# Optimization experiments

Hardware: AMD Instinct MI355X
Metric: run time of the kernel (lower is better)

The kernel has to match this reference:

```python
import jax, jax.numpy as jnp
import numpy as np

B, H, W, C = 2, 48, 48, 768
HEADS, HD = 12, 64
MLP = 3072
BOT = 384


def ln(x, w, b, eps=1e-5):
    mu = x.mean(-1, keepdims=True)
    var = ((x - mu) ** 2).mean(-1, keepdims=True)
    return (x - mu) * jax.lax.rsqrt(var + eps) * w + b


def ln_chan(x, w, b, eps=1e-6):
    # detectron2-style LayerNorm over channel dim for NCHW tensors
    mu = x.mean(1, keepdims=True)
    var = ((x - mu) ** 2).mean(1, keepdims=True)
    return (x - mu) * jax.lax.rsqrt(var + eps) * w[None, :, None, None] + b[None, :, None, None]


def conv(x, w, pad):
    return jax.lax.conv_general_dilated(x, w, (1, 1), [(pad, pad), (pad, pad)],
                                        dimension_numbers=('NCHW', 'OIHW', 'NCHW'))


def setup_inputs() -> dict:
    key = jax.random.key(0)
    ks = jax.random.split(key, 32)
    r = lambda i, shape, s=0.02: (jax.random.normal(ks[i], shape) * s).astype(jnp.float32)
    return {
        'x': jax.random.normal(ks[0], (B, H, W, C), dtype=jnp.float32),
        'norm1_w': jnp.ones((C,), jnp.float32), 'norm1_b': jnp.zeros((C,), jnp.float32),
        'qkv_w': r(1, (C, 3 * C)), 'qkv_b': r(2, (3 * C,)),
        'proj_w': r(3, (C, C)), 'proj_b': r(4, (C,)),
        'rel_pos_h': r(5, (2 * H - 1, HD)), 'rel_pos_w': r(6, (2 * W - 1, HD)),
        'norm2_w': jnp.ones((C,), jnp.float32), 'norm2_b': jnp.zeros((C,), jnp.float32),
        'fc1_w': r(7, (C, MLP)), 'fc1_b': r(8, (MLP,)),
        'fc2_w': r(9, (MLP, C)), 'fc2_b': r(10, (C,)),
        'conv1_w': r(11, (BOT, C, 1, 1)), 'rln1_w': jnp.ones((BOT,), jnp.float32), 'rln1_b': jnp.zeros((BOT,), jnp.float32),
        'conv2_w': r(12, (BOT, BOT, 3, 3)), 'rln2_w': jnp.ones((BOT,), jnp.float32), 'rln2_b': jnp.zeros((BOT,), jnp.float32),
        'conv3_w': r(13, (C, BOT, 1, 1)), 'rln3_w': r(14, (C,)), 'rln3_b': r(15, (C,)),
    }


def reference(x, norm1_w, norm1_b, qkv_w, qkv_b, proj_w, proj_b, rel_pos_h, rel_pos_w,
              norm2_w, norm2_b, fc1_w, fc1_b, fc2_w, fc2_b,
              conv1_w, rln1_w, rln1_b, conv2_w, rln2_w, rln2_b, conv3_w, rln3_w, rln3_b):
    b, h, w, c = x.shape
    hd = c // HEADS
    n = h * w
    scale = hd ** -0.5

    shortcut = x
    xn = ln(x, norm1_w, norm1_b)
    # qkv projection: (B,N,3,heads,hd) -> (3, B*heads, N, hd)
    qkv = (xn.reshape(b, n, c) @ qkv_w + qkv_b).reshape(b, n, 3, HEADS, hd)
    qkv = qkv.transpose(2, 0, 3, 1, 4).reshape(3, b * HEADS, n, hd)
    q, k, v = qkv[0], qkv[1], qkv[2]

    attn = jnp.einsum('bnd,bmd->bnm', q * scale, k)  # (B*heads, N, N)

    # decomposed relative position bias
    idx_h = jnp.arange(h)[:, None] - jnp.arange(h)[None, :] + (h - 1)
    idx_w = jnp.arange(w)[:, None] - jnp.arange(w)[None, :] + (w - 1)
    Rh = rel_pos_h[idx_h]  # (H, H, hd)
    Rw = rel_pos_w[idx_w]  # (W, W, hd)
    rq = q.reshape(b * HEADS, h, w, hd)
    rel_h = jnp.einsum('bhwc,hkc->bhwk', rq, Rh)
    rel_w = jnp.einsum('bhwc,wkc->bhwk', rq, Rw)
    attn = attn.reshape(b * HEADS, h, w, h, w) + rel_h[:, :, :, :, None] + rel_w[:, :, :, None, :]
    attn = jax.nn.softmax(attn.reshape(b * HEADS, n, n), axis=-1)

    out = (attn @ v).reshape(b, HEADS, h, w, hd).transpose(0, 2, 3, 1, 4).reshape(b, h, w, c)
    x = shortcut + (out @ proj_w + proj_b)

    # MLP
    xn = ln(x, norm2_w, norm2_b)
    hdn = jax.nn.gelu(xn @ fc1_w + fc1_b, approximate=False)
    x = x + (hdn @ fc2_w + fc2_b)

    # residual bottleneck block (NCHW)
    y = x.transpose(0, 3, 1, 2)
    o = jax.nn.gelu(ln_chan(conv(y, conv1_w, 0), rln1_w, rln1_b), approximate=False)
    o = jax.nn.gelu(ln_chan(conv(o, conv2_w, 1), rln2_w, rln2_b), approximate=False)
    o = ln_chan(conv(o, conv3_w, 0), rln3_w, rln3_b)
    y = y + o
    return y.transpose(0, 2, 3, 1)
```

## Files before the change

### kernel.cpp

```cpp
#include <hip/hip_runtime.h>

typedef unsigned short ushort_t;
typedef __attribute__((ext_vector_type(8))) short bf16x8;
typedef __attribute__((ext_vector_type(4))) float f32x4;

#define DEV static __device__ __forceinline__

DEV ushort_t f2bf(float f){
  union { float f; unsigned u; } v; v.f = f;
  unsigned r = v.u + 0x7FFFu + ((v.u >> 16) & 1u);
  return (ushort_t)(r >> 16);
}
DEV float bf2f(ushort_t h){
  union { unsigned u; float f; } v; v.u = ((unsigned)h) << 16;
  return v.f;
}
DEV float gelu_f(float x){ return 0.5f * x * (1.f + erff(x * 0.70710678118654752f)); }

#define MFMA16(a,b,c) __builtin_amdgcn_mfma_f32_16x16x32_bf16((a),(b),(c),0,0,0)

DEV void gld16(const ushort_t* g, ushort_t* l){
  __builtin_amdgcn_global_load_lds(
      (const __attribute__((address_space(1))) unsigned int*)g,
      (__attribute__((address_space(3))) unsigned int*)l, 16, 0, 0);
}


__global__ __launch_bounds__(256) void transpose_all_kernel(
    const float* __restrict__ s0, const float* __restrict__ s1,
    const float* __restrict__ s2, const float* __restrict__ s3,
    ushort_t* __restrict__ d0, ushort_t* __restrict__ d1,
    ushort_t* __restrict__ d2, ushort_t* __restrict__ d3){
  __shared__ float tile[32][33];
  int b = blockIdx.x;
  const float* src; ushort_t* dst; int K, N, bx, by;
  if(b < 1728){ src=s0; dst=d0; K=768;  N=2304; bx=b%24;          by=b/24; }
  else if(b < 2304){ int c=b-1728; src=s1; dst=d1; K=768;  N=768;  bx=c%24; by=c/24; }
  else if(b < 4608){ int c=b-2304; src=s2; dst=d2; K=768;  N=3072; bx=c%24; by=c/24; }
  else             { int c=b-4608; src=s3; dst=d3; K=3072; N=768;  bx=c%96; by=c/96; }
  int k0 = bx*32, n0 = by*32;
  int tx = threadIdx.x & 31, ty = threadIdx.x >> 5;
  #pragma unroll
  for(int i = ty; i < 32; i += 8) tile[i][tx] = src[(long)(k0+i)*N + n0 + tx];
  __syncthreads();
  #pragma unroll
  for(int i = ty; i < 32; i += 8) dst[(long)(n0+i)*K + k0 + tx] = f2bf(tile[tx][i]);
}

__global__ void cast_all_kernel(
    const float* __restrict__ c1w, const float* __restrict__ c2w,
    const float* __restrict__ c3w, const float* __restrict__ rph,
    const float* __restrict__ rpw,
    ushort_t* __restrict__ wc1, ushort_t* __restrict__ wc2,
    ushort_t* __restrict__ wc3, ushort_t* __restrict__ tabh,
    ushort_t* __restrict__ tabw){
  int i = blockIdx.x*256 + threadIdx.x;
  if(i < 294912){ wc1[i] = f2bf(c1w[i]); }
  else if(i < 1622016){
    int j = i - 294912;
    int co = j / 3456, r = j - co*3456;
    int dy = r / 1152; int r2 = r - dy*1152;
    int dx = r2 / 384; int ci = r2 - dx*384;
    wc2[j] = f2bf(c2w[((co*384 + ci)*3 + dy)*3 + dx]);
  }
  else if(i < 1916928){ int j = i - 1622016; wc3[j] = f2bf(c3w[j]); }
  else if(i < 1923008){ int j = i - 1916928; tabh[j] = f2bf(rph[j]); }
  else if(i < 1929088){ int j = i - 1923008; tabw[j] = f2bf(rpw[j]); }
}

__global__ __launch_bounds__(256) void vt_kernel(
    const ushort_t* __restrict__ v, ushort_t* __restrict__ vt){
  __shared__ __align__(16) ushort_t t[64][72];
  int bh = blockIdx.y, nt = blockIdx.x;
  int tid = threadIdx.x;
  #pragma unroll
  for(int p=0;p<2;p++){
    int item = tid + p*256;
    int tok = item >> 3, ch = item & 7;
    bf16x8 vv = *(const bf16x8*)(v + ((long)(bh*2304 + nt*64 + tok))*64 + ch*8);
    #pragma unroll
    for(int j=0;j<8;j++) t[ch*8+j][tok] = (ushort_t)vv[j];
  }
  __syncthreads();
  #pragma unroll
  for(int p=0;p<2;p++){
    int item = tid + p*256;
    int d = item >> 3, c2 = item & 7;
    bf16x8 rd = *(const bf16x8*)&t[d][c2*8];
    *(bf16x8*)(vt + ((long)(bh*64 + d))*2304 + nt*64 + c2*8) = rd;
  }
}

template<int D, bool GELU, bool RES, bool PADOUT>
__global__ __launch_bounds__(256) void ln_kernel(
    const float* __restrict__ in, const float* __restrict__ w, const float* __restrict__ bv,
    const float* __restrict__ res, float eps,
    ushort_t* __restrict__ outb, float* __restrict__ outf){
  constexpr int PER = D/64;
  int lane = threadIdx.x & 63, wid = threadIdx.x >> 6;
  long row = (long)blockIdx.x*4 + wid;
  const float* ip = in + row*D;
  float x[PER]; float s = 0.f;
  #pragma unroll
  for(int i=0;i<PER;i++){ x[i] = ip[i*64 + lane]; s += x[i]; }
  #pragma unroll
  for(int o=32;o>=1;o>>=1) s += __shfl_xor(s, o);
  float mu = s * (1.f/D);
  float vs = 0.f;
  #pragma unroll
  for(int i=0;i<PER;i++){ float d = x[i]-mu; vs += d*d; }
  #pragma unroll
  for(int o=32;o>=1;o>>=1) vs += __shfl_xor(vs, o);
  float rstd = rsqrtf(vs*(1.f/D) + eps);
  long obase;
  if constexpr(PADOUT){
    int bb = (int)(row / 2304); int rm = (int)(row - (long)bb*2304);
    int y = rm / 48, xx = rm - y*48;
    obase = ((long)((bb*50 + y+1)*50) + (xx+1))*384;
  } else obase = row*D;
  #pragma unroll
  for(int i=0;i<PER;i++){
    int c = i*64 + lane;
    float y = (x[i]-mu)*rstd*w[c] + bv[c];
    if constexpr(GELU) y = gelu_f(y);
    if constexpr(RES)  y += res[row*D + c];
    if(outb) outb[obase + c] = f2bf(y);
    if(outf) outf[row*D + c] = y;
  }
}

__global__ __launch_bounds__(256) void relpos_mfma_kernel(
    const ushort_t* __restrict__ q, const ushort_t* __restrict__ tabh,
    const ushort_t* __restrict__ tabw,
    float* __restrict__ relh, float* __restrict__ relw){
  const int bh = blockIdx.y;
  const bool isH = (blockIdx.z == 0);
  const int w = threadIdx.x >> 6, lane = threadIdx.x & 63;
  const int la = lane & 15, grp = lane >> 4;
  const int pos0 = blockIdx.x*4 + w;
  const ushort_t* tab = isH ? tabh : tabw;
  float* outp = isH ? relh : relw;
  const ushort_t* qbase = q + (long)bh*2304*64;

  bf16x8 bf0[3], bf1[3];
  #pragma unroll
  for(int ni=0;ni<3;ni++){
    int dpos = pos0 - (ni*16+la) + 47;
    const ushort_t* tp = tab + dpos*64 + grp*8;
    bf0[ni] = *(const bf16x8*)tp;
    bf1[ni] = *(const bf16x8*)(tp+32);
  }
  #pragma unroll
  for(int mi=0;mi<3;mi++){
    int arow = mi*16 + la;
    long na = isH ? ((long)pos0*48 + arow) : ((long)arow*48 + pos0);
    const ushort_t* qp = qbase + na*64 + grp*8;
    bf16x8 a0 = *(const bf16x8*)qp;
    bf16x8 a1 = *(const bf16x8*)(qp+32);
    f32x4 c[3];
    #pragma unroll
    for(int ni=0;ni<3;ni++){
      f32x4 z; z[0]=0.f; z[1]=0.f; z[2]=0.f; z[3]=0.f;
      z = MFMA16(a0, bf0[ni], z);
      z = MFMA16(a1, bf1[ni], z);
      c[ni] = z;
    }
    #pragma unroll
    for(int ni=0;ni<3;ni++)
      #pragma unroll
      for(int r=0;r<4;r++){
        int orow = mi*16 + grp*4 + r;
        long no = isH ? ((long)pos0*48 + orow) : ((long)orow*48 + pos0);
        outp[((long)bh*2304 + no)*48 + ni*16 + la] = c[ni][r] * 8.0f;
      }
  }
}

template<int BM, int BN, int EPI, bool IM2COL>
__global__ __launch_bounds__(256) void gemm_kernel(
    const ushort_t* __restrict__ A, const ushort_t* __restrict__ Wt,
    const float* __restrict__ bias, const float* __restrict__ res,
    float* __restrict__ outf, ushort_t* __restrict__ ob0,
    ushort_t* __restrict__ ob1, ushort_t* __restrict__ ob2,
    int N, int Kdim){
  constexpr int FRm = BM/32, FRn = BN/32;
  __shared__ __align__(16) ushort_t Asm[BM*64];
  __shared__ __align__(16) ushort_t Bsm[BN*64];
  const int tid = threadIdx.x, lane = tid & 63, w = tid >> 6;
  const int wm = w >> 1, wn = w & 1;
  const int la = lane & 15, grp = lane >> 4;
  const int m0 = blockIdx.y * BM, n0 = blockIdx.x * BN;
  f32x4 acc[FRm][FRn];
  #pragma unroll
  for(int i=0;i<FRm;i++)
    #pragma unroll
    for(int j=0;j<FRn;j++)
      #pragma unroll
      for(int r=0;r<4;r++) acc[i][j][r] = 0.f;

  const int srw = lane >> 3;
  const int scs = ((lane&7) ^ srw) * 8;
  for(int k0 = 0; k0 < Kdim; k0 += 64){
    if(k0) __syncthreads();
    #pragma unroll
    for(int t=0;t<FRm;t++){
      int r = w*(BM/4) + t*8 + srw;
      const ushort_t* ga;
      if constexpr(IM2COL){
        int m = m0 + r;
        int bb = m / 2304; int rm = m - bb*2304;
        int y = rm / 48, x = rm - y*48;
        int dy = k0 / 1152; int r2 = k0 - dy*1152;
        int dx = r2 / 384;  int cb = r2 - dx*384;
        ga = A + (((long)((bb*50 + y+dy)*50) + (x+dx))*384 + cb + scs);
      } else {
        ga = A + (long)(m0+r)*Kdim + k0 + scs;
      }
      gld16(ga, &Asm[(w*(BM/4)+t*8)*64]);
    }
    #pragma unroll
    for(int t=0;t<FRn;t++){
      int r = w*(BN/4) + t*8 + srw;
      gld16(Wt + (long)(n0+r)*Kdim + k0 + scs, &Bsm[(w*(BN/4)+t*8)*64]);
    }
    __syncthreads();
    #pragma unroll
    for(int ks=0; ks<2; ks++){
      bf16x8 af[FRm], bfm[FRn];
      #pragma unroll
      for(int mi=0;mi<FRm;mi++){
        int row = wm*(BM/2) + mi*16 + la;
        af[mi] = *(const bf16x8*)&Asm[row*64 + ((((ks<<2)+grp) ^ (row&7))*8)];
      }
      #pragma unroll
      for(int ni=0;ni<FRn;ni++){
        int row = wn*(BN/2) + ni*16 + la;
        bfm[ni] = *(const bf16x8*)&Bsm[row*64 + ((((ks<<2)+grp) ^ (row&7))*8)];
      }
      #pragma unroll
      for(int mi=0;mi<FRm;mi++)
        #pragma unroll
        for(int ni=0;ni<FRn;ni++)
          acc[mi][ni] = MFMA16(af[mi], bfm[ni], acc[mi][ni]);
    }
  }
  #pragma unroll
  for(int mi=0;mi<FRm;mi++)
  #pragma unroll
  for(int ni=0;ni<FRn;ni++)
  #pragma unroll
  for(int r=0;r<4;r++){
    int mm = m0 + wm*(BM/2) + mi*16 + grp*4 + r;
    int nn = n0 + wn*(BN/2) + ni*16 + la;
    float v = acc[mi][ni][r];
    if constexpr(EPI == 0){
      outf[(long)mm*N + nn] = v;
    } else if constexpr(EPI == 1){
      v += bias[nn];
      int s = nn / 768; int rem = nn - s*768;
      int head = rem >> 6, d = rem & 63;
      if(s == 0) v *= 0.125f;
      int bb = mm / 2304; int nloc = mm - bb*2304;
      long idx = ((long)((bb*12+head)*2304 + nloc))*64 + d;
      ushort_t hv = f2bf(v);
      if(s == 0) ob0[idx] = hv; else if(s == 1) ob1[idx] = hv; else ob2[idx] = hv;
    } else if constexpr(EPI == 2){
      v += bias[nn] + res[(long)mm*N + nn];
      outf[(long)mm*N + nn] = v;
    } else if constexpr(EPI == 3){
      v = gelu_f(v + bias[nn]);
      ob0[(long)mm*N + nn] = f2bf(v);
    } else if constexpr(EPI == 4){
      v += bias[nn] + res[(long)mm*N + nn];
      outf[(long)mm*N + nn] = v;
      ob0[(long)mm*N + nn] = f2bf(v);
    }
  }
}

#define NSPLIT 2
#define NTS 18
__global__ __launch_bounds__(512) void attn_kernel(
    const ushort_t* __restrict__ Q, const ushort_t* __restrict__ Kb,
    const ushort_t* __restrict__ VT, const float* __restrict__ relh,
    const float* __restrict__ relw, float* __restrict__ Opart,
    float* __restrict__ mpart, float* __restrict__ lpart){
  __shared__ __align__(16) ushort_t Kl[2][64*64];
  __shared__ __align__(16) ushort_t Vl[2][64*64];
  const int bh = blockIdx.y, qt = blockIdx.x, sp = blockIdx.z;
  const int tid = threadIdx.x, lane = tid & 63, w = tid >> 6;
  const int la = lane & 15, grp = lane >> 4;
  const int qg = qt*128 + w*16 + la;
  const long row = (long)bh*2304 + qg;
  const int key0 = sp*NTS*64;

  const ushort_t* qp = Q + row*64 + grp*8;
  const bf16x8 qa0 = *(const bf16x8*)qp;
  const bf16x8 qa1 = *(const bf16x8*)(qp + 32);

  const ushort_t* kg = Kb + ((long)bh*2304 + key0)*64;
  const ushort_t* vg = VT + (long)bh*64*2304 + key0;
  const float* rhq = relh + row*48;

  f32x4 rw4[3];
  {
    const float* rwq = relw + row*48 + grp*4;
    #pragma unroll
    for(int c=0;c<3;c++) rw4[c] = *(const f32x4*)(rwq + 16*c);
  }

  const int srw = lane >> 3;
  const int scs = ((lane&7) ^ srw) * 8;
  const int strow = w*8 + srw;

  f32x4 acc[4];
  #pragma unroll
  for(int nf=0;nf<4;nf++){ acc[nf][0]=0.f; acc[nf][1]=0.f; acc[nf][2]=0.f; acc[nf][3]=0.f; }
  float m_run = -3e38f, l_run = 0.f;

  gld16(kg + (long)strow*64 + scs, &Kl[0][(w*8)*64]);
  gld16(vg + (long)strow*2304 + scs, &Vl[0][(w*8)*64]);

  for(int t=0; t<6; t++){
    #define ATTN_ITER(u)                                                         \
    {                                                                            \
      const int j = 3*t + (u);                                                   \
      const int cur = (t + (u)) & 1;                                             \
      asm volatile("s_waitcnt vmcnt(0)" ::: "memory");                           \
      __builtin_amdgcn_sched_barrier(0);                                         \
      __builtin_amdgcn_s_barrier();                                              \
      __builtin_amdgcn_sched_barrier(0);                                         \
      const int h0 = sp*24 + 4*t + (u);                                          \
      const float rha = rhq[h0];                                                 \
      const float rhb = rhq[h0+1];                                               \
      if(j+1 < NTS){                                                             \
        gld16(kg + ((long)((j+1)*64 + strow))*64 + scs, &Kl[cur^1][(w*8)*64]);   \
        gld16(vg + (long)strow*2304 + (j+1)*64 + scs, &Vl[cur^1][(w*8)*64]);     \
      }                                                                          \
      f32x4 s[4];                                                                \
      _Pragma("unroll")                                                          \
      for(int nf=0;nf<4;nf++){                                                   \
        const ushort_t* kl = &Kl[cur][(nf*16+la)*64];                            \
        bf16x8 k0 = *(const bf16x8*)(kl + ((grp ^ (la&7))*8));                   \
        bf16x8 k1 = *(const bf16x8*)(kl + (((4+grp) ^ (la&7))*8));               \
        f32x4 z; z[0]=0.f; z[1]=0.f; z[2]=0.f; z[3]=0.f;                         \
        z = MFMA16(k0, qa0, z);                                                  \
        z = MFMA16(k1, qa1, z);                                                  \
        s[nf] = z;                                                               \
      }                                                                          \
      float lmax = -3e38f;                                                       \
      _Pragma("unroll")                                                          \
      for(int nf=0;nf<4;nf++){                                                   \
        const int cp = (u) + nf;                                                 \
        const float rh = (cp >= 3) ? rhb : rha;                                  \
        const int c = (cp >= 3) ? cp-3 : cp;                                     \
        _Pragma("unroll")                                                        \
        for(int r=0;r<4;r++){                                                    \
          s[nf][r] += rh + rw4[c][r];                                            \
          lmax = fmaxf(lmax, s[nf][r]);                                          \
        }                                                                        \
      }                                                                          \
      lmax = fmaxf(lmax, __shfl_xor(lmax,16));                                   \
      lmax = fmaxf(lmax, __shfl_xor(lmax,32));                                   \
      if(!__all(lmax <= m_run + 8.f)){                                           \
        const float mnew = fmaxf(m_run, lmax);                                   \
        const float alpha = __expf(m_run - mnew);                                \
        m_run = mnew;                                                            \
        l_run *= alpha;                                                          \
        _Pragma("unroll")                                                        \
        for(int nf=0;nf<4;nf++)                                                  \
          _Pragma("unroll")                                                      \
          for(int r=0;r<4;r++) acc[nf][r] *= alpha;                              \
      }                                                                          \
      float psum = 0.f;                                                          \
      _Pragma("unroll")                                                          \
      for(int nf=0;nf<4;nf++)                                                    \
        _Pragma("unroll")                                                        \
        for(int r=0;r<4;r++){                                                    \
          s[nf][r] = __expf(s[nf][r] - m_run);                                   \
          psum += s[nf][r];                                                      \
        }                                                                        \
      psum += __shfl_xor(psum,16);                                               \
      psum += __shfl_xor(psum,32);                                               \
      l_run += psum;                                                             \
      unsigned pk[4][2];                                                         \
      _Pragma("unroll")                                                          \
      for(int nf=0;nf<4;nf++)                                                    \
        _Pragma("unroll")                                                        \
        for(int h=0;h<2;h++)                                                     \
          asm("v_cvt_pk_bf16_f32 %0, %1, %2"                                     \
              : "=v"(pk[nf][h]) : "v"(s[nf][2*h]), "v"(s[nf][2*h+1]));           \
      _Pragma("unroll")                                                          \
      for(int ks=0; ks<2; ks++){                                                 \
        unsigned wd[4];                                                          \
        _Pragma("unroll")                                                        \
        for(int j2=0;j2<4;j2++){                                                 \
          int src = la + 16*(((grp&1)<<1) + (j2>>1));                            \
          unsigned wA = __shfl(pk[2*ks  ][j2&1], src);                           \
          unsigned wB = __shfl(pk[2*ks+1][j2&1], src);                           \
          wd[j2] = (grp >= 2) ? wB : wA;                                         \
        }                                                                        \
        union { unsigned uu[4]; bf16x8 v; } pa;                                  \
        pa.uu[0]=wd[0]; pa.uu[1]=wd[1]; pa.uu[2]=wd[2]; pa.uu[3]=wd[3];          \
        _Pragma("unroll")                                                        \
        for(int nf=0;nf<4;nf++){                                                 \
          const ushort_t* vl = &Vl[cur][(nf*16+la)*64];                          \
          bf16x8 vb = *(const bf16x8*)(vl + ((((ks<<2)+grp) ^ (la&7))*8));       \
          acc[nf] = MFMA16(vb, pa.v, acc[nf]);                                   \
        }                                                                        \
      }                                                                          \
    }
    ATTN_ITER(0)
    ATTN_ITER(1)
    ATTN_ITER(2)
    #undef ATTN_ITER
  }

  float* op = Opart + ((long)sp*55296 + row)*64;
  #pragma unroll
  for(int nf=0;nf<4;nf++)
    *(f32x4*)(op + nf*16 + grp*4) = acc[nf];
  if(grp == 0){
    mpart[(long)sp*55296 + row] = m_run;
    lpart[(long)sp*55296 + row] = l_run;
  }
}

__global__ __launch_bounds__(256) void attn_merge_kernel(
    const float* __restrict__ Opart, const float* __restrict__ mpart,
    const float* __restrict__ lpart, ushort_t* __restrict__ outp){
  int wid = threadIdx.x >> 6, lane = threadIdx.x & 63;
  long row = (long)blockIdx.x*4 + wid;
  int bh = (int)(row / 2304); int n = (int)(row - (long)bh*2304);
  int b = bh / 12, head = bh - b*12;
  float m0 = mpart[row], m1 = mpart[55296+row];
  float ms = fmaxf(m0, m1);
  float w0 = __expf(m0-ms), w1 = __expf(m1-ms);
  float l = w0*lpart[row] + w1*lpart[55296+row];
  float o = w0*Opart[row*64+lane] + w1*Opart[(55296+row)*64+lane];
  outp[((long)b*2304+n)*768 + head*64 + lane] = f2bf(o / l);
}

extern "C" void kernel_launch(void* const* d_in, const int* in_sizes, int n_in,
                              void* d_out, int out_size, void* d_ws, size_t ws_size,
                              hipStream_t stream){
  const float* x     = (const float*)d_in[0];
  const float* n1w   = (const float*)d_in[1];
  const float* n1b   = (const float*)d_in[2];
  const float* qkvw  = (const float*)d_in[3];
  const float* qkvb  = (const float*)d_in[4];
  const float* projw = (const float*)d_in[5];
  const float* projb = (const float*)d_in[6];
  const float* rph   = (const float*)d_in[7];
  const float* rpw   = (const float*)d_in[8];
  const float* n2w   = (const float*)d_in[9];
  const float* n2b   = (const float*)d_in[10];
  const float* fc1w  = (const float*)d_in[11];
  const float* fc1b  = (const float*)d_in[12];
  const float* fc2w  = (const float*)d_in[13];
  const float* fc2b  = (const float*)d_in[14];
  const float* c1w   = (const float*)d_in[15];
  const float* r1w   = (const float*)d_in[16];
  const float* r1b   = (const float*)d_in[17];
  const float* c2w   = (const float*)d_in[18];
  const float* r2w   = (const float*)d_in[19];
  const float* r2b   = (const float*)d_in[20];
  const float* c3w   = (const float*)d_in[21];
  const float* r3w   = (const float*)d_in[22];
  const float* r3b   = (const float*)d_in[23];
  float* out = (float*)d_out;

  char* base = (char*)d_ws;
  size_t off = 0;
  auto carve = [&](size_t bytes)->char*{
    char* p = base + off;
    off += (bytes + 255) & ~(size_t)255;
    return p;
  };
  const long T = 4608;

  ushort_t* wqkvT = (ushort_t*)carve((size_t)2304*768*2);
  ushort_t* wprojT= (ushort_t*)carve((size_t)768*768*2);
  ushort_t* wfc1T = (ushort_t*)carve((size_t)3072*768*2);
  ushort_t* wfc2T = (ushort_t*)carve((size_t)768*3072*2);
  ushort_t* wc1   = (ushort_t*)carve((size_t)384*768*2);
  ushort_t* wc2   = (ushort_t*)carve((size_t)384*3456*2);
  ushort_t* wc3   = (ushort_t*)carve((size_t)768*384*2);
  ushort_t* tabhb = (ushort_t*)carve((size_t)95*64*2);
  ushort_t* tabwb = (ushort_t*)carve((size_t)95*64*2);
  ushort_t* xn1   = (ushort_t*)carve((size_t)T*768*2);
  ushort_t* qb    = (ushort_t*)carve((size_t)24*2304*64*2);
  ushort_t* kbuf  = (ushort_t*)carve((size_t)24*2304*64*2);
  ushort_t* vbuf  = (ushort_t*)carve((size_t)24*2304*64*2);
  ushort_t* vbufT = (ushort_t*)carve((size_t)24*2304*64*2);
  float*    relh  = (float*)carve((size_t)24*2304*48*4);
  float*    relw  = (float*)carve((size_t)24*2304*48*4);
  float*    Opart = (float*)carve((size_t)2*55296*64*4);
  float*    mpart = (float*)carve((size_t)2*55296*4);
  float*    lpart = (float*)carve((size_t)2*55296*4);
  ushort_t* attno = (ushort_t*)carve((size_t)T*768*2);
  float*    x1    = (float*)carve((size_t)T*768*4);
  ushort_t* xn2   = (ushort_t*)carve((size_t)T*768*2);
  ushort_t* hmlp  = (ushort_t*)carve((size_t)T*3072*2);
  float*    x2    = (float*)carve((size_t)T*768*4);
  ushort_t* x2b   = (ushort_t*)carve((size_t)T*768*2);
  float*    c1    = (float*)carve((size_t)T*384*4);
  ushort_t* o1pad = (ushort_t*)carve((size_t)2*50*50*384*2);
  float*    c2    = (float*)carve((size_t)T*384*4);
  ushort_t* o2    = (ushort_t*)carve((size_t)T*384*2);
  float*    c3    = (float*)carve((size_t)T*768*4);
  (void)ws_size; (void)in_sizes; (void)n_in; (void)out_size;

  transpose_all_kernel<<<dim3(6912),256,0,stream>>>(qkvw, projw, fc1w, fc2w,
                                                    wqkvT, wprojT, wfc1T, wfc2T);
  cast_all_kernel<<<dim3(7536),256,0,stream>>>(c1w, c2w, c3w, rph, rpw,
                                               wc1, wc2, wc3, tabhb, tabwb);
  hipMemsetAsync(o1pad, 0, (size_t)2*50*50*384*2, stream);

  ln_kernel<768,false,false,false><<<dim3(1152),256,0,stream>>>(x, n1w, n1b, nullptr, 1e-5f, xn1, nullptr);
  gemm_kernel<128,128,1,false><<<dim3(18,36),256,0,stream>>>(xn1, wqkvT, qkvb, nullptr, nullptr, qb, kbuf, vbuf, 2304, 768);
  vt_kernel<<<dim3(36,24),256,0,stream>>>(vbuf, vbufT);
  relpos_mfma_kernel<<<dim3(12,24,2),256,0,stream>>>(qb, tabhb, tabwb, relh, relw);
  attn_kernel<<<dim3(18,24,2),512,0,stream>>>(qb, kbuf, vbufT, relh, relw, Opart, mpart, lpart);
  attn_merge_kernel<<<dim3(13824),256,0,stream>>>(Opart, mpart, lpart, attno);
  gemm_kernel<64,128,2,false><<<dim3(6,72),256,0,stream>>>(attno, wprojT, projb, x, x1, nullptr, nullptr, nullptr, 768, 768);
  ln_kernel<768,false,false,false><<<dim3(1152),256,0,stream>>>(x1, n2w, n2b, nullptr, 1e-5f, xn2, nullptr);
  gemm_kernel<128,128,3,false><<<dim3(24,36),256,0,stream>>>(xn2, wfc1T, fc1b, nullptr, nullptr, hmlp, nullptr, nullptr, 3072, 768);
  gemm_kernel<64,128,4,false><<<dim3(6,72),256,0,stream>>>(hmlp, wfc2T, fc2b, x1, x2, x2b, nullptr, nullptr, 768, 3072);
  gemm_kernel<64,128,0,false><<<dim3(3,72),256,0,stream>>>(x2b, wc1, nullptr, nullptr, c1, nullptr, nullptr, nullptr, 384, 768);
  ln_kernel<384,true,false,true><<<dim3(1152),256,0,stream>>>(c1, r1w, r1b, nullptr, 1e-6f, o1pad, nullptr);
  gemm_kernel<64,128,0,true><<<dim3(3,72),256,0,stream>>>(o1pad, wc2, nullptr, nullptr, c2, nullptr, nullptr, nullptr, 384, 3456);
  ln_kernel<384,true,false,false><<<dim3(1152),256,0,stream>>>(c2, r2w, r2b, nullptr, 1e-6f, o2, nullptr);
  gemm_kernel<64,128,0,false><<<dim3(6,72),256,0,stream>>>(o2, wc3, nullptr, nullptr, c3, nullptr, nullptr, nullptr, 768, 384);
  ln_kernel<768,false,true,false><<<dim3(1152),256,0,stream>>>(c3, r3w, r3b, x2, 1e-6f, nullptr, out);
}
```

Before: 444.4 us.

## Process two query fragments per wave in attention and shrink GEMM N-tiles

```diff
diff --git a/kernel.cpp b/kernel.cpp
--- a/kernel.cpp
+++ b/kernel.cpp
@@ -170,7 +170,7 @@
       #pragma unroll
       for(int r=0;r<4;r++){
         int orow = mi*16 + grp*4 + r;
-        long no = isH ? ((long)pos0*48 + orow) : ((long)orow*48 + pos0);
+        long no = isH ? ((long)pos0*48 + orow) : ((long)arow*0 + (long)orow*48 + pos0);
         outp[((long)bh*2304 + no)*48 + ni*16 + la] = c[ni][r] * 8.0f;
       }
   }
@@ -280,7 +280,7 @@
 
 #define NSPLIT 2
 #define NTS 18
-__global__ __launch_bounds__(512) void attn_kernel(
+__global__ __launch_bounds__(256) void attn_kernel(
     const ushort_t* __restrict__ Q, const ushort_t* __restrict__ Kb,
     const ushort_t* __restrict__ VT, const float* __restrict__ relh,
     const float* __restrict__ relw, float* __restrict__ Opart,
@@ -290,139 +290,183 @@
   const int bh = blockIdx.y, qt = blockIdx.x, sp = blockIdx.z;
   const int tid = threadIdx.x, lane = tid & 63, w = tid >> 6;
   const int la = lane & 15, grp = lane >> 4;
-  const int qg = qt*128 + w*16 + la;
-  const long row = (long)bh*2304 + qg;
+  const long row0 = (long)bh*2304 + qt*128 + w*16 + la;
+  const long row1 = row0 + 64;
   const int key0 = sp*NTS*64;
 
-  const ushort_t* qp = Q + row*64 + grp*8;
-  const bf16x8 qa0 = *(const bf16x8*)qp;
-  const bf16x8 qa1 = *(const bf16x8*)(qp + 32);
+  const ushort_t* qp0 = Q + row0*64 + grp*8;
+  const bf16x8 qa0_0 = *(const bf16x8*)qp0;
+  const bf16x8 qa1_0 = *(const bf16x8*)(qp0 + 32);
+  const ushort_t* qp1 = Q + row1*64 + grp*8;
+  const bf16x8 qa0_1 = *(const bf16x8*)qp1;
+  const bf16x8 qa1_1 = *(const bf16x8*)(qp1 + 32);
 
   const ushort_t* kg = Kb + ((long)bh*2304 + key0)*64;
   const ushort_t* vg = VT + (long)bh*64*2304 + key0;
-  const float* rhq = relh + row*48;
-
-  f32x4 rw4[3];
+  const float* rhq0 = relh + row0*48;
+  const float* rhq1 = relh + row1*48;
+
+  f32x4 rw4_0[3], rw4_1[3];
   {
-    const float* rwq = relw + row*48 + grp*4;
-    #pragma unroll
-    for(int c=0;c<3;c++) rw4[c] = *(const f32x4*)(rwq + 16*c);
+    const float* rwq0 = relw + row0*48 + grp*4;
+    const float* rwq1 = relw + row1*48 + grp*4;
+    #pragma unroll
+    for(int c=0;c<3;c++){
+      rw4_0[c] = *(const f32x4*)(rwq0 + 16*c);
+      rw4_1[c] = *(const f32x4*)(rwq1 + 16*c);
+    }
   }
 
   const int srw = lane >> 3;
   const int scs = ((lane&7) ^ srw) * 8;
-  const int strow = w*8 + srw;
-
-  f32x4 acc[4];
-  #pragma unroll
-  for(int nf=0;nf<4;nf++){ acc[nf][0]=0.f; acc[nf][1]=0.f; acc[nf][2]=0.f; acc[nf][3]=0.f; }
-  float m_run = -3e38f, l_run = 0.f;
-
-  gld16(kg + (long)strow*64 + scs, &Kl[0][(w*8)*64]);
-  gld16(vg + (long)strow*2304 + scs, &Vl[0][(w*8)*64]);
+
+  f32x4 acc0[4], acc1[4];
+  #pragma unroll
+  for(int nf=0;nf<4;nf++)
+    #pragma unroll
+    for(int r=0;r<4;r++){ acc0[nf][r]=0.f; acc1[nf][r]=0.f; }
+  float m0r = -3e38f, l0r = 0.f, m1r = -3e38f, l1r = 0.f;
+
+  #pragma unroll
+  for(int tt=0;tt<2;tt++){
+    int r = w*16 + tt*8 + srw;
+    gld16(kg + (long)r*64 + scs, &Kl[0][(w*16+tt*8)*64]);
+    gld16(vg + (long)r*2304 + scs, &Vl[0][(w*16+tt*8)*64]);
+  }
+
+  #define SOFTMAX_FRAG(S, ACC, MR, LR, PK, RHA, RHB, RW)                       \
+  {                                                                            \
+    float lmax = -3e38f;                                                       \
+    _Pragma("unroll")                                                          \
+    for(int nf=0;nf<4;nf++){                                                   \
+      const int cp = CURU + nf;                                                \
+      const float rh = (cp >= 3) ? (RHB) : (RHA);                              \
+      const int c = (cp >= 3) ? cp-3 : cp;                                     \
+      _Pragma("unroll")                                                        \
+      for(int r=0;r<4;r++){                                                    \
+        S[nf][r] += rh + RW[c][r];                                             \
+        lmax = fmaxf(lmax, S[nf][r]);                                          \
+      }                                                                        \
+    }                                                                          \
+    lmax = fmaxf(lmax, __shfl_xor(lmax,16));                                   \
+    lmax = fmaxf(lmax, __shfl_xor(lmax,32));                                   \
+    if(!__all(lmax <= MR + 8.f)){                                              \
+      const float mnew = fmaxf(MR, lmax);                                      \
+      const float alpha = __expf(MR - mnew);                                   \
+      MR = mnew; LR *= alpha;                                                  \
+      _Pragma("unroll")                                                        \
+      for(int nf=0;nf<4;nf++)                                                  \
+        _Pragma("unroll")                                                      \
+        for(int r=0;r<4;r++) ACC[nf][r] *= alpha;                              \
+    }                                                                          \
+    float psum = 0.f;                                                          \
+    _Pragma("unroll")                                                          \
+    for(int nf=0;nf<4;nf++)                                                    \
+      _Pragma("unroll")                                                        \
+      for(int r=0;r<4;r++){                                                    \
+        S[nf][r] = __expf(S[nf][r] - MR);                                      \
+        psum += S[nf][r];                                                      \
+      }                                                                        \
+    psum += __shfl_xor(psum,16);                                               \
+    psum += __shfl_xor(psum,32);                                               \
+    LR += psum;                                                                \
+    _Pragma("unroll")                                                          \
+    for(int nf=0;nf<4;nf++)                                                    \
+      _Pragma("unroll")                                                        \
+      for(int h=0;h<2;h++)                                                     \
+        asm("v_cvt_pk_bf16_f32 %0, %1, %2"                                     \
+            : "=v"(PK[nf][h]) : "v"(S[nf][2*h]), "v"(S[nf][2*h+1]));           \
+  }
+
+  #define MAKE_PA(PK, KS, PA)                                                  \
+  {                                                                            \
+    unsigned wd[4];                                                            \
+    _Pragma("unroll")                                                          \
+    for(int j2=0;j2<4;j2++){                                                   \
+      int src = la + 16*(((grp&1)<<1) + (j2>>1));                              \
+      unsigned wA = __shfl(PK[2*(KS)  ][j2&1], src);                           \
+      unsigned wB = __shfl(PK[2*(KS)+1][j2&1], src);                           \
+      wd[j2] = (grp >= 2) ? wB : wA;                                           \
+    }                                                                          \
+    PA.uu[0]=wd[0]; PA.uu[1]=wd[1]; PA.uu[2]=wd[2]; PA.uu[3]=wd[3];            \
+  }
 
   for(int t=0; t<6; t++){
-    #define ATTN_ITER(u)                                                         \
-    {                                                                            \
-      const int j = 3*t + (u);                                                   \
-      const int cur = (t + (u)) & 1;                                             \
-      asm volatile("s_waitcnt vmcnt(0)" ::: "memory");                           \
-      __builtin_amdgcn_sched_barrier(0);                                         \
-      __builtin_amdgcn_s_barrier();                                              \
-      __builtin_amdgcn_sched_barrier(0);                                         \
-      const int h0 = sp*24 + 4*t + (u);                                          \
-      const float rha = rhq[h0];                                                 \
-      const float rhb = rhq[h0+1];                                               \
-      if(j+1 < NTS){                                                             \
-        gld16(kg + ((long)((j+1)*64 + strow))*64 + scs, &Kl[cur^1][(w*8)*64]);   \
-        gld16(vg + (long)strow*2304 + (j+1)*64 + scs, &Vl[cur^1][(w*8)*64]);     \
-      }                                                                          \
-      f32x4 s[4];                                                                \
-      _Pragma("unroll")                                                          \
-      for(int nf=0;nf<4;nf++){                                                   \
-        const ushort_t* kl = &Kl[cur][(nf*16+la)*64];                            \
-        bf16x8 k0 = *(const bf16x8*)(kl + ((grp ^ (la&7))*8));                   \
-        bf16x8 k1 = *(const bf16x8*)(kl + (((4+grp) ^ (la&7))*8));               \
-        f32x4 z; z[0]=0.f; z[1]=0.f; z[2]=0.f; z[3]=0.f;                         \
-        z = MFMA16(k0, qa0, z);                                                  \
-        z = MFMA16(k1, qa1, z);                                                  \
-        s[nf] = z;                                                               \
-      }                                                                          \
-      float lmax = -3e38f;                                                       \
-      _Pragma("unroll")                                                          \
-      for(int nf=0;nf<4;nf++){                                                   \
-        const int cp = (u) + nf;                                                 \
-        const float rh = (cp >= 3) ? rhb : rha;                                  \
-        const int c = (cp >= 3) ? cp-3 : cp;                                     \
-        _Pragma("unroll")                                                        \
-        for(int r=0;r<4;r++){                                                    \
-          s[nf][r] += rh + rw4[c][r];                                            \
-          lmax = fmaxf(lmax, s[nf][r]);                                          \
-        }                                                                        \
-      }                                                                          \
-      lmax = fmaxf(lmax, __shfl_xor(lmax,16));                                   \
-      lmax = fmaxf(lmax, __shfl_xor(lmax,32));                                   \
-      if(!__all(lmax <= m_run + 8.f)){                                           \
-        const float mnew = fmaxf(m_run, lmax);                                   \
-        const float alpha = __expf(m_run - mnew);                                \
-        m_run = mnew;                                                            \
-        l_run *= alpha;                                                          \
-        _Pragma("unroll")                                                        \
-        for(int nf=0;nf<4;nf++)                                                  \
-          _Pragma("unroll")                                                      \
-          for(int r=0;r<4;r++) acc[nf][r] *= alpha;                              \
-      }                                                                          \
-      float psum = 0.f;                                                          \
-      _Pragma("unroll")                                                          \
-      for(int nf=0;nf<4;nf++)                                                    \
-        _Pragma("unroll")                                                        \
-        for(int r=0;r<4;r++){                                                    \
-          s[nf][r] = __expf(s[nf][r] - m_run);                                   \
-          psum += s[nf][r];                                                      \
-        }                                                                        \
-      psum += __shfl_xor(psum,16);                                               \
-      psum += __shfl_xor(psum,32);                                               \
-      l_run += psum;                                                             \
-      unsigned pk[4][2];                                                         \
-      _Pragma("unroll")                                                          \
-      for(int nf=0;nf<4;nf++)                                                    \
-        _Pragma("unroll")                                                        \
-        for(int h=0;h<2;h++)                                                     \
-          asm("v_cvt_pk_bf16_f32 %0, %1, %2"                                     \
-              : "=v"(pk[nf][h]) : "v"(s[nf][2*h]), "v"(s[nf][2*h+1]));           \
-      _Pragma("unroll")                                                          \
-      for(int ks=0; ks<2; ks++){                                                 \
-        unsigned wd[4];                                                          \
-        _Pragma("unroll")                                                        \
-        for(int j2=0;j2<4;j2++){                                                 \
-          int src = la + 16*(((grp&1)<<1) + (j2>>1));                            \
-          unsigned wA = __shfl(pk[2*ks  ][j2&1], src);                           \
-          unsigned wB = __shfl(pk[2*ks+1][j2&1], src);                           \
-          wd[j2] = (grp >= 2) ? wB : wA;                                         \
-        }                                                                        \
-        union { unsigned uu[4]; bf16x8 v; } pa;                                  \
-        pa.uu[0]=wd[0]; pa.uu[1]=wd[1]; pa.uu[2]=wd[2]; pa.uu[3]=wd[3];          \
-        _Pragma("unroll")                                                        \
-        for(int nf=0;nf<4;nf++){                                                 \
-          const ushort_t* vl = &Vl[cur][(nf*16+la)*64];                          \
-          bf16x8 vb = *(const bf16x8*)(vl + ((((ks<<2)+grp) ^ (la&7))*8));       \
-          acc[nf] = MFMA16(vb, pa.v, acc[nf]);                                   \
-        }                                                                        \
-      }                                                                          \
-    }
+    #define ATTN_ITER(u)                                                       \
+    {                                                                          \
+      const int j = 3*t + (u);                                                 \
+      const int cur = (t + (u)) & 1;                                           \
+      asm volatile("s_waitcnt vmcnt(0)" ::: "memory");                         \
+      __builtin_amdgcn_sched_barrier(0);                                       \
+      __builtin_amdgcn_s_barrier();                                            \
+      __builtin_amdgcn_sched_barrier(0);                                       \
+      const int h0 = sp*24 + 4*t + (u);                                        \
+      const float rha0 = rhq0[h0], rhb0 = rhq0[h0+1];                          \
+      const float rha1 = rhq1[h0], rhb1 = rhq1[h0+1];                          \
+      if(j+1 < NTS){                                                           \
+        _Pragma("unroll")                                                      \
+        for(int tt=0;tt<2;tt++){                                               \
+          int r = w*16 + tt*8 + srw;                                           \
+          gld16(kg + ((long)((j+1)*64 + r))*64 + scs, &Kl[cur^1][(w*16+tt*8)*64]); \
+          gld16(vg + (long)r*2304 + (j+1)*64 + scs, &Vl[cur^1][(w*16+tt*8)*64]);   \
+        }                                                                      \
+      }                                                                        \
+      f32x4 s0[4], s1[4];                                                      \
+      _Pragma("unroll")                                                        \
+      for(int nf=0;nf<4;nf++){                                                 \
+        const ushort_t* kl = &Kl[cur][(nf*16+la)*64];                          \
+        bf16x8 k0 = *(const bf16x8*)(kl + ((grp ^ (la&7))*8));                 \
+        bf16x8 k1 = *(const bf16x8*)(kl + (((4+grp) ^ (la&7))*8));             \
+        f32x4 z; z[0]=0.f; z[1]=0.f; z[2]=0.f; z[3]=0.f;                       \
+        z = MFMA16(k0, qa0_0, z);                                              \
+        z = MFMA16(k1, qa1_0, z);                                              \
+        s0[nf] = z;                                                            \
+        f32x4 y; y[0]=0.f; y[1]=0.f; y[2]=0.f; y[3]=0.f;                       \
+        y = MFMA16(k0, qa0_1, y);                                              \
+        y = MFMA16(k1, qa1_1, y);                                              \
+        s1[nf] = y;                                                            \
+      }                                                                        \
+      unsigned pk0[4][2], pk1[4][2];                                           \
+      SOFTMAX_FRAG(s0, acc0, m0r, l0r, pk0, rha0, rhb0, rw4_0)                 \
+      SOFTMAX_FRAG(s1, acc1, m1r, l1r, pk1, rha1, rhb1, rw4_1)                 \
+      _Pragma("unroll")                                                        \
+      for(int ks=0; ks<2; ks++){                                               \
+        union { unsigned uu[4]; bf16x8 v; } pa0, pa1;                          \
+        MAKE_PA(pk0, ks, pa0)                                                  \
+        MAKE_PA(pk1, ks, pa1)                                                  \
+        _Pragma("unroll")                                                      \
+        for(int nf=0;nf<4;nf++){                                               \
+          const ushort_t* vl = &Vl[cur][(nf*16+la)*64];                        \
+          bf16x8 vb = *(const bf16x8*)(vl + ((((ks<<2)+grp) ^ (la&7))*8));     \
+          acc0[nf] = MFMA16(vb, pa0.v, acc0[nf]);                              \
+          acc1[nf] = MFMA16(vb, pa1.v, acc1[nf]);                              \
+        }                                                                      \
+      }                                                                        \
+    }
+    #define CURU 0
     ATTN_ITER(0)
+    #undef CURU
+    #define CURU 1
     ATTN_ITER(1)
+    #undef CURU
+    #define CURU 2
     ATTN_ITER(2)
+    #undef CURU
     #undef ATTN_ITER
   }
 
-  float* op = Opart + ((long)sp*55296 + row)*64;
-  #pragma unroll
-  for(int nf=0;nf<4;nf++)
-    *(f32x4*)(op + nf*16 + grp*4) = acc[nf];
+  float* op0 = Opart + ((long)sp*55296 + row0)*64;
+  float* op1 = Opart + ((long)sp*55296 + row1)*64;
+  #pragma unroll
+  for(int nf=0;nf<4;nf++){
+    *(f32x4*)(op0 + nf*16 + grp*4) = acc0[nf];
+    *(f32x4*)(op1 + nf*16 + grp*4) = acc1[nf];
+  }
   if(grp == 0){
-    mpart[(long)sp*55296 + row] = m_run;
-    lpart[(long)sp*55296 + row] = l_run;
+    mpart[(long)sp*55296 + row0] = m0r;
+    lpart[(long)sp*55296 + row0] = l0r;
+    mpart[(long)sp*55296 + row1] = m1r;
+    lpart[(long)sp*55296 + row1] = l1r;
   }
 }
 
@@ -521,16 +565,16 @@
   gemm_kernel<128,128,1,false><<<dim3(18,36),256,0,stream>>>(xn1, wqkvT, qkvb, nullptr, nullptr, qb, kbuf, vbuf, 2304, 768);
   vt_kernel<<<dim3(36,24),256,0,stream>>>(vbuf, vbufT);
   relpos_mfma_kernel<<<dim3(12,24,2),256,0,stream>>>(qb, tabhb, tabwb, relh, relw);
-  attn_kernel<<<dim3(18,24,2),512,0,stream>>>(qb, kbuf, vbufT, relh, relw, Opart, mpart, lpart);
+  attn_kernel<<<dim3(18,24,2),256,0,stream>>>(qb, kbuf, vbufT, relh, relw, Opart, mpart, lpart);
   attn_merge_kernel<<<dim3(13824),256,0,stream>>>(Opart, mpart, lpart, attno);
-  gemm_kernel<64,128,2,false><<<dim3(6,72),256,0,stream>>>(attno, wprojT, projb, x, x1, nullptr, nullptr, nullptr, 768, 768);
+  gemm_kernel<64,64,2,false><<<dim3(12,72),256,0,stream>>>(attno, wprojT, projb, x, x1, nullptr, nullptr, nullptr, 768, 768);
   ln_kernel<768,false,false,false><<<dim3(1152),256,0,stream>>>(x1, n2w, n2b, nullptr, 1e-5f, xn2, nullptr);
   gemm_kernel<128,128,3,false><<<dim3(24,36),256,0,stream>>>(xn2, wfc1T, fc1b, nullptr, nullptr, hmlp, nullptr, nullptr, 3072, 768);
-  gemm_kernel<64,128,4,false><<<dim3(6,72),256,0,stream>>>(hmlp, wfc2T, fc2b, x1, x2, x2b, nullptr, nullptr, 768, 3072);
-  gemm_kernel<64,128,0,false><<<dim3(3,72),256,0,stream>>>(x2b, wc1, nullptr, nullptr, c1, nullptr, nullptr, nullptr, 384, 768);
+  gemm_kernel<64,64,4,false><<<dim3(12,72),256,0,stream>>>(hmlp, wfc2T, fc2b, x1, x2, x2b, nullptr, nullptr, 768, 3072);
+  gemm_kernel<64,64,0,false><<<dim3(6,72),256,0,stream>>>(x2b, wc1, nullptr, nullptr, c1, nullptr, nullptr, nullptr, 384, 768);
   ln_kernel<384,true,false,true><<<dim3(1152),256,0,stream>>>(c1, r1w, r1b, nullptr, 1e-6f, o1pad, nullptr);
-  gemm_kernel<64,128,0,true><<<dim3(3,72),256,0,stream>>>(o1pad, wc2, nullptr, nullptr, c2, nullptr, nullptr, nullptr, 384, 3456);
+  gemm_kernel<64,64,0,true><<<dim3(6,72),256,0,stream>>>(o1pad, wc2, nullptr, nullptr, c2, nullptr, nullptr, nullptr, 384, 3456);
   ln_kernel<384,true,false,false><<<dim3(1152),256,0,stream>>>(c2, r2w, r2b, nullptr, 1e-6f, o2, nullptr);
-  gemm_kernel<64,128,0,false><<<dim3(6,72),256,0,stream>>>(o2, wc3, nullptr, nullptr, c3, nullptr, nullptr, nullptr, 768, 384);
+  gemm_kernel<64,64,0,false><<<dim3(12,72),256,0,stream>>>(o2, wc3, nullptr, nullptr, c3, nullptr, nullptr, nullptr, 768, 384);
   ln_kernel<768,false,true,false><<<dim3(1152),256,0,stream>>>(c3, r3w, r3b, x2, 1e-6f, nullptr, out);
 }
```

After: 444.8 us. About the same (+0.1%).
